# Optimization experiments

Measured on AMD Instinct MI355X. Metric: run time of the kernel, lower is better.

The kernel has to match this reference:

```python
import jax, jax.numpy as jnp
import numpy as np

HEADS = 8
TOK = 4  # num_query_tokens
EPS = 1e-5


def _ln(x, w, b):
    mu = jnp.mean(x, -1, keepdims=True)
    v = jnp.var(x, -1, keepdims=True)
    return (x - mu) / jnp.sqrt(v + EPS) * w + b


def _inorm(x):
    # InstanceNorm3d(affine=False): normalize per (B,C) over spatial dims
    mu = jnp.mean(x, (2, 3, 4), keepdims=True)
    v = jnp.var(x, (2, 3, 4), keepdims=True)
    return (x - mu) / jnp.sqrt(v + EPS)


def _conv3(x, w, b):
    y = jax.lax.conv_general_dilated(x, w, (1, 1, 1), 'SAME',
                                     dimension_numbers=('NCDHW', 'OIDHW', 'NCDHW'))
    return y + b[None, :, None, None, None]


def setup_inputs() -> dict:
    key = jax.random.key(0)
    ks = jax.random.split(key, 8)
    B, C, D, H, W = 4, 320, 16, 32, 32
    CLI = 320
    QD = C * TOK  # 1280
    s = 0.02
    return {
        'img_feat': jax.random.normal(ks[0], (B, C, D, H, W), jnp.float32),
        'cli_feat': jax.random.normal(ks[1], (B, CLI), jnp.float32),
        'Wq': jax.random.normal(ks[2], (QD, CLI), jnp.float32) * s,
        'bq': jnp.zeros((QD,), jnp.float32),
        'lnq_w': jnp.ones((QD,), jnp.float32),
        'lnq_b': jnp.zeros((QD,), jnp.float32),
        'Wk': jax.random.normal(ks[3], (C, C), jnp.float32) * s,
        'bk': jnp.zeros((C,), jnp.float32),
        'Wv': jax.random.normal(ks[4], (C, C), jnp.float32) * s,
        'bv': jnp.zeros((C,), jnp.float32),
        'Wo': jax.random.normal(ks[5], (C, QD), jnp.float32) * s,
        'bo': jnp.zeros((C,), jnp.float32),
        'lno_w': jnp.ones((C,), jnp.float32),
        'lno_b': jnp.zeros((C,), jnp.float32),
        'Wf1': jax.random.normal(ks[6], (C, 2 * C, 3, 3, 3), jnp.float32) * s,
        'bf1': jnp.zeros((C,), jnp.float32),
        'Wf2': jax.random.normal(ks[7], (C, C, 3, 3, 3), jnp.float32) * s,
        'bf2': jnp.zeros((C,), jnp.float32),
    }


def reference(img_feat, cli_feat, Wq, bq, lnq_w, lnq_b, Wk, bk, Wv, bv,
              Wo, bo, lno_w, lno_b, Wf1, bf1, Wf2, bf2):
    B, C, D, H, W = img_feat.shape
    S = D * H * W
    hd = C // HEADS
    scale = hd ** -0.5
    # clinical features -> 4 query tokens per head: [B, heads, head_dim, TOK]
    q = _ln(cli_feat @ Wq.T + bq, lnq_w, lnq_b).reshape(B, HEADS, hd, TOK)
    # 1x1x1 convs == per-position linear over channels
    x = img_feat.reshape(B, C, S)
    k = (jnp.einsum('oc,bcs->bos', Wk, x) + bk[None, :, None]).reshape(B, HEADS, hd, S)
    v = (jnp.einsum('oc,bcs->bos', Wv, x) + bv[None, :, None]).reshape(B, HEADS, hd, S)
    # [B, heads, TOK, S] scores -> softmax over spatial
    attn = jax.nn.softmax(jnp.einsum('bhdt,bhds->bhts', q, k) * scale, axis=-1)
    # value @ attn^T -> [B, heads, head_dim, TOK], flatten like torch .view(B,-1)
    o = jnp.einsum('bhds,bhts->bhdt', v, attn).reshape(B, HEADS * hd * TOK)
    o = _ln(o @ Wo.T + bo, lno_w, lno_b)  # [B, C]
    bcast = jnp.broadcast_to(o[:, :, None, None, None], (B, C, D, H, W))
    fused = jnp.concatenate([img_feat, bcast], axis=1)  # [B, 2C, D, H, W]
    h = jax.nn.gelu(_inorm(_conv3(fused, Wf1, bf1)), approximate=False)
    h = _inorm(_conv3(h, Wf2, bf2))
    return h + img_feat
```

## Files before the change

kernel.cpp:

```cpp
#include <hip/hip_runtime.h>
#include <hip/hip_bf16.h>
#include <math.h>

typedef unsigned short u16;

#define DEV static __device__ __forceinline__

DEV float bfu(u16 u) { union { unsigned int i; float f; } v; v.i = ((unsigned int)u) << 16; return v.f; }
DEV u16 fbu(float f) { __hip_bfloat16 h = __float2bfloat16(f); return *reinterpret_cast<u16*>(&h); }

template <typename T> struct ModeOf;
template <> struct ModeOf<u16>   { static constexpr int v = 0; };
template <> struct ModeOf<float> { static constexpr int v = 1; };
template <typename T> DEV float ld(const void* p, size_t i);
template <> DEV float ld<u16>(const void* p, size_t i)   { return bfu(((const u16*)p)[i]); }
template <> DEV float ld<float>(const void* p, size_t i) { return ((const float*)p)[i]; }

template <typename T> DEV float dot8(const void* img, size_t idx, const float* ar, int s);
template <> DEV float dot8<u16>(const void* img, size_t idx, const float* ar, int s) {
    uint4 v = *reinterpret_cast<const uint4*>((const u16*)img + idx + s);
    const float4 a0 = *reinterpret_cast<const float4*>(ar + s);
    const float4 a1 = *reinterpret_cast<const float4*>(ar + s + 4);
    return a0.x*bfu(v.x & 0xffff) + a0.y*bfu(v.x >> 16)
         + a0.z*bfu(v.y & 0xffff) + a0.w*bfu(v.y >> 16)
         + a1.x*bfu(v.z & 0xffff) + a1.y*bfu(v.z >> 16)
         + a1.z*bfu(v.w & 0xffff) + a1.w*bfu(v.w >> 16);
}
template <> DEV float dot8<float>(const void* img, size_t idx, const float* ar, int s) {
    const float4 x0 = *reinterpret_cast<const float4*>((const float*)img + idx + s);
    const float4 x1 = *reinterpret_cast<const float4*>((const float*)img + idx + s + 4);
    const float4 a0 = *reinterpret_cast<const float4*>(ar + s);
    const float4 a1 = *reinterpret_cast<const float4*>(ar + s + 4);
    return a0.x*x0.x + a0.y*x0.y + a0.z*x0.z + a0.w*x0.w
         + a1.x*x1.x + a1.y*x1.y + a1.z*x1.z + a1.w*x1.w;
}

#define NB 4
#define NC 320
#define ND 16
#define NH 32
#define NW 32
#define NS 16384
#define NHD 40
#define NQD 1280
#define NR 32
#define NTOK 4
#define OUT_N (NB*NC*NS)
#define EPSV 1e-5f
#define SCALE 0.15811388300841898f

#define YKS 8
#define YCH (NS / YKS)

#define CSL 32
#define NSL 10
#define HALO_D 4
#define HALO_H 6
#define PIXW 34
#define NPIX (HALO_D*HALO_H*PIXW)
#define PACKN (27*10*20*64*8)

typedef __attribute__((ext_vector_type(8))) short bf16x8;
typedef __attribute__((ext_vector_type(4))) float f32x4;

DEV int swz4(int p) { return (p + (p >> 2)) & 3; }

DEV float blk_sum(float v, float* red) {
    __syncthreads();
#pragma unroll
    for (int o = 32; o > 0; o >>= 1) v += __shfl_down(v, o, 64);
    int wv = threadIdx.x >> 6, ln = threadIdx.x & 63;
    if (ln == 0) red[wv] = v;
    __syncthreads();
    return red[0] + red[1] + red[2] + red[3];
}
DEV float blk_max(float v, float* red) {
    __syncthreads();
#pragma unroll
    for (int o = 32; o > 0; o >>= 1) v = fmaxf(v, __shfl_down(v, o, 64));
    int wv = threadIdx.x >> 6, ln = threadIdx.x & 63;
    if (ln == 0) red[wv] = v;
    __syncthreads();
    return fmaxf(fmaxf(red[0], red[1]), fmaxf(red[2], red[3]));
}

__global__ void detect_kernel(const u16* __restrict__ lnqw, int* __restrict__ flag) {
    if (threadIdx.x == 0) flag[0] = (lnqw[0] == 0x3F80) ? 0 : 1;
}

template <typename T>
__global__ __launch_bounds__(256) void q_kernel(const int* __restrict__ flag,
        const void* __restrict__ cli, const void* __restrict__ Wq, const void* __restrict__ bq,
        const void* __restrict__ lnw, const void* __restrict__ lnb, float* __restrict__ qout) {
    if (*flag != ModeOf<T>::v) return;
    int b = blockIdx.x, tid = threadIdx.x;
    __shared__ float cl[NC];
    __shared__ float red[8];
    for (int i = tid; i < NC; i += 256) cl[i] = ld<T>(cli, b * NC + i);
    __syncthreads();
    float loc[5];
    float s1 = 0.f, s2 = 0.f;
#pragma unroll
    for (int k = 0; k < 5; ++k) {
        int j = tid + k * 256;
        float a = ld<T>(bq, j);
        size_t wr = (size_t)j * NC;
        for (int c = 0; c < NC; ++c) a += cl[c] * ld<T>(Wq, wr + c);
        loc[k] = a; s1 += a; s2 += a * a;
    }
    s1 = blk_sum(s1, red);
    s2 = blk_sum(s2, red);
    float mu = s1 / (float)NQD;
    float var = fmaxf(s2 / (float)NQD - mu * mu, 0.f);
    float rs = rsqrtf(var + EPSV);
#pragma unroll
    for (int k = 0; k < 5; ++k) {
        int j = tid + k * 256;
        qout[(size_t)b * NQD + j] = (loc[k] - mu) * rs * ld<T>(lnw, j) + ld<T>(lnb, j);
    }
}

template <typename T>
__global__ __launch_bounds__(256) void qw_kernel(const int* __restrict__ flag,
        const float* __restrict__ q, const void* __restrict__ Wk, const void* __restrict__ bk,
        float* __restrict__ qW, float* __restrict__ qb, u16* __restrict__ qwb) {
    if (*flag != ModeOf<T>::v) return;
    int gid = blockIdx.x * 256 + threadIdx.x;
    if (gid < NB * NR * NC) {
        int c = gid % NC;
        int r = (gid / NC) % NR;
        int b = gid / (NC * NR);
        int h = r >> 2, t = r & 3;
        float a = 0.f;
        const float* qb_ = q + (size_t)b * NQD;
        for (int d = 0; d < NHD; ++d)
            a += qb_[(h * NHD + d) * NTOK + t] * ld<T>(Wk, (size_t)(h * NHD + d) * NC + c);
        qW[gid] = a;
        int kk = c >> 5, gg = (c >> 3) & 3, j = c & 7;
        int mf = r >> 4, lane = (gg << 4) | (r & 15);
        qwb[(((size_t)(b * 10 + kk) * 2 + mf) << 9) + (lane << 3) + j] = fbu(a);
    }
    if (gid < NB * NR) {
        int r = gid & 31, b = gid >> 5;
        int h = r >> 2, t = r & 3;
        float a = 0.f;
        const float* qb_ = q + (size_t)b * NQD;
        for (int d = 0; d < NHD; ++d)
            a += qb_[(h * NHD + d) * NTOK + t] * ld<T>(bk, h * NHD + d);
        qb[gid] = a;
    }
}

__global__ __launch_bounds__(256) void scores_mm_kernel(
        const u16* __restrict__ imgt, const u16* __restrict__ qwb,
        const float* __restrict__ qb, float* __restrict__ attn) {
    int b = blockIdx.y;
    int s0 = blockIdx.x * 256 + (threadIdx.x >> 6) * 64;
    int ln = threadIdx.x & 63;
    int col = ln & 15, g = ln >> 4;
    bf16x8 af[10][2];
    const u16* qa = qwb + (size_t)b * 10 * 2 * 512;
#pragma unroll
    for (int kk = 0; kk < 10; ++kk)
#pragma unroll
        for (int mf = 0; mf < 2; ++mf)
            af[kk][mf] = *reinterpret_cast<const bf16x8*>(qa + (((kk << 1) + mf) << 9) + (ln << 3));
    f32x4 acc[2][4];
#pragma unroll
    for (int mf = 0; mf < 2; ++mf)
#pragma unroll
        for (int nf = 0; nf < 4; ++nf) acc[mf][nf] = (f32x4){0.f, 0.f, 0.f, 0.f};
    const u16* xb = imgt + (size_t)b * NS * NC;
#pragma unroll
    for (int kk = 0; kk < 10; ++kk) {
#pragma unroll
        for (int nf = 0; nf < 4; ++nf) {
            bf16x8 bf = *reinterpret_cast<const bf16x8*>(
                xb + (size_t)(s0 + nf * 16 + col) * NC + kk * 32 + (g << 3));
#pragma unroll
            for (int mf = 0; mf < 2; ++mf)
                acc[mf][nf] = __builtin_amdgcn_mfma_f32_16x16x32_bf16(
                    af[kk][mf], bf, acc[mf][nf], 0, 0, 0);
        }
    }
#pragma unroll
    for (int mf = 0; mf < 2; ++mf)
#pragma unroll
        for (int nf = 0; nf < 4; ++nf)
#pragma unroll
            for (int r = 0; r < 4; ++r) {
                int row = mf * 16 + g * 4 + r;
                attn[((size_t)(b * NR + row) << 14) + s0 + nf * 16 + col] =
                    (acc[mf][nf][r] + qb[b * NR + row]) * SCALE;
            }
}

__global__ __launch_bounds__(256) void softmax_kernel(float* __restrict__ attn) {
    int row = blockIdx.x;
    float* rp = attn + ((size_t)row << 14);
    __shared__ float red[8];
    float m = -1e30f;
    for (int s = threadIdx.x; s < NS; s += 256) m = fmaxf(m, rp[s]);
    m = blk_max(m, red);
    float sum = 0.f;
    for (int s = threadIdx.x; s < NS; s += 256) {
        float e = expf(rp[s] - m);
        rp[s] = e; sum += e;
    }
    sum = blk_sum(sum, red);
    float inv = 1.f / sum;
    for (int s = threadIdx.x; s < NS; s += 256) rp[s] *= inv;
}

template <typename T>
__global__ __launch_bounds__(256) void y_kernel(const int* __restrict__ flag,
        const float* __restrict__ attn, const void* __restrict__ img, float* __restrict__ yp) {
    if (*flag != ModeOf<T>::v) return;
    int row = blockIdx.x;
    int ks  = blockIdx.y;
    int b = row >> 5;
    int wv = threadIdx.x >> 6, ln = threadIdx.x & 63;
    const float* ar = attn + ((size_t)row << 14) + ks * YCH;
    size_t xb = (size_t)b * NC * NS + ks * YCH;
    float* yout = yp + ((size_t)ks * NB * NR + row) * NC;
    for (int c = wv; c < NC; c += 4) {
        size_t xr = xb + ((size_t)c << 14);
        float p = 0.f;
#pragma unroll
        for (int it = 0; it < YCH / 512; ++it)
            p += dot8<T>(img, xr, ar, it * 512 + ln * 8);
#pragma unroll
        for (int o = 32; o > 0; o >>= 1) p += __shfl_down(p, o, 64);
        if (ln == 0) yout[c] = p;
    }
}

__global__ __launch_bounds__(256) void yred_kernel(const float* __restrict__ yp, float* __restrict__ y) {
    int i = blockIdx.x * 256 + threadIdx.x;
    if (i >= NB * NR * NC) return;
    float s = 0.f;
#pragma unroll
    for (int k = 0; k < YKS; ++k) s += yp[(size_t)k * NB * NR * NC + i];
    y[i] = s;
}

template <typename T>
__global__ __launch_bounds__(256) void o_kernel(const int* __restrict__ flag,
        const float* __restrict__ y, const void* __restrict__ Wv, const void* __restrict__ bv,
        const void* __restrict__ Wo, const void* __restrict__ bo,
        const void* __restrict__ lnw, const void* __restrict__ lnb, float* __restrict__ o2) {
    if (*flag != ModeOf<T>::v) return;
    int b = blockIdx.x, tid = threadIdx.x;
    __shared__ float yl[NR * NC];
    __shared__ float ol[NQD];
    __shared__ float red[8];
    for (int i = tid; i < NR * NC; i += 256) yl[i] = y[(size_t)b * NR * NC + i];
    __syncthreads();
#pragma unroll
    for (int k = 0; k < 5; ++k) {
        int i = tid + k * 256;
        int h = i / 160, rem = i - h * 160;
        int d = rem >> 2, t = rem & 3;
        int wr = h * NHD + d, r = h * NTOK + t;
        float a = ld<T>(bv, wr);
        size_t wvr = (size_t)wr * NC;
        const float* yr = yl + r * NC;
        for (int c = 0; c < NC; ++c) a += ld<T>(Wv, wvr + c) * yr[c];
        ol[i] = a;
    }
    __syncthreads();
    for (int j = tid; j < NC; j += 256) {
        float a = ld<T>(bo, j);
        size_t wor = (size_t)j * NQD;
        for (int i = 0; i < NQD; ++i) a += ld<T>(Wo, wor + i) * ol[i];
        yl[j] = a;
    }
    __syncthreads();
    float s1 = 0.f, s2 = 0.f;
    for (int j = tid; j < NC; j += 256) { float v = yl[j]; s1 += v; s2 += v * v; }
    s1 = blk_sum(s1, red);
    s2 = blk_sum(s2, red);
    float mu = s1 / (float)NC;
    float var = fmaxf(s2 / (float)NC - mu * mu, 0.f);
    float rs = rsqrtf(var + EPSV);
    for (int j = tid; j < NC; j += 256)
        o2[(size_t)b * NC + j] = (yl[j] - mu) * rs * ld<T>(lnw, j) + ld<T>(lnb, j);
}

template <typename T>
__global__ __launch_bounds__(256) void p_kernel(const int* __restrict__ flag,
        const float* __restrict__ o2, const void* __restrict__ Wf1, float* __restrict__ P) {
    if (*flag != ModeOf<T>::v) return;
    int o = blockIdx.x, b = blockIdx.y;
    int tid = threadIdx.x, wv = tid >> 6, ln = tid & 63;
    __shared__ float red[4 * 27];
    __shared__ float taps[27];
    float acc[27];
#pragma unroll
    for (int k = 0; k < 27; ++k) acc[k] = 0.f;
    for (int c = tid; c < NC; c += 256) {
        float oc = o2[(size_t)b * NC + c];
        size_t wp = ((size_t)o * 640 + 320 + c) * 27;
#pragma unroll
        for (int k = 0; k < 27; ++k) acc[k] += oc * ld<T>(Wf1, wp + k);
    }
#pragma unroll
    for (int k = 0; k < 27; ++k) {
        float v = acc[k];
#pragma unroll
        for (int off = 32; off > 0; off >>= 1) v += __shfl_down(v, off, 64);
        if (ln == 0) red[wv * 27 + k] = v;
    }
    __syncthreads();
    if (tid < 27) taps[tid] = red[tid] + red[27 + tid] + red[54 + tid] + red[81 + tid];
    __syncthreads();
    if (tid < 27) {
        int pd = tid / 9, ph = (tid / 3) % 3, pw = tid % 3;
        float s = 0.f;
        for (int kd = 0; kd < 3; ++kd) {
            if ((pd == 0 && kd == 0) || (pd == 2 && kd == 2)) continue;
            for (int kh = 0; kh < 3; ++kh) {
                if ((ph == 0 && kh == 0) || (ph == 2 && kh == 2)) continue;
                for (int kw = 0; kw < 3; ++kw) {
                    if ((pw == 0 && kw == 0) || (pw == 2 && kw == 2)) continue;
                    s += taps[kd * 9 + kh * 3 + kw];
                }
            }
        }
        P[(size_t)(b * NC + o) * 27 + tid] = s;
    }
}

template <typename T>
__global__ __launch_bounds__(256) void imgt_kernel(const int* __restrict__ flag,
        const void* __restrict__ img, u16* __restrict__ outT) {
    if (*flag != ModeOf<T>::v) return;
    int b = blockIdx.z, c0 = blockIdx.y << 5, s0 = blockIdx.x << 5;
    int r = threadIdx.x >> 3, c4 = (threadIdx.x & 7) << 2;
    __shared__ float tile[32][33];
#pragma unroll
    for (int j = 0; j < 4; ++j)
        tile[r][c4 + j] = ld<T>(img, ((size_t)(b * NC + c0 + r) << 14) + s0 + c4 + j);
    __syncthreads();
    u16* op = outT + ((size_t)b * NS + s0 + r) * NC + c0 + c4;
#pragma unroll
    for (int j = 0; j < 4; ++j) op[j] = fbu(tile[c4 + j][r]);
}

template <typename TW>
__global__ __launch_bounds__(256) void pack_kernel(const int* __restrict__ flag,
        const void* __restrict__ wgt, const void* __restrict__ bias,
        u16* __restrict__ wpack, float* __restrict__ biasf, int wic) {
    if (*flag != ModeOf<TW>::v) return;
    int gid = blockIdx.x * 256 + threadIdx.x;
    if (gid < NC) biasf[gid] = ld<TW>(bias, gid);
    int lane = gid & 63;
    int rest = gid >> 6;
    int obg = rest % 20;  rest /= 20;
    int t = rest % 27;    int cs = rest / 27;
    int o  = (obg << 4) + (lane & 15);
    int c0 = (cs << 5) + ((lane >> 4) << 3);
    u16* dst = wpack + (size_t)gid * 8;
#pragma unroll
    for (int j = 0; j < 8; ++j)
        dst[j] = fbu(ld<TW>(wgt, ((size_t)o * wic + c0 + j) * 27 + t));
}

__global__ __launch_bounds__(256, 3) void convmm_kernel(
        const u16* __restrict__ inT, const u16* __restrict__ wpack,
        const float* __restrict__ biasf, const float* __restrict__ Pp,
        u16* __restrict__ out) {
    int d0 = (blockIdx.x >> 3) << 1;
    int h0 = (blockIdx.x & 7) << 2;
    int ob = blockIdx.y;
    int b  = blockIdx.z;
    int tid = threadIdx.x;
    int wv = tid >> 6, ln = tid & 63;
    int col = ln & 15, g = ln >> 4;

    __shared__ __align__(16) u16 lin[NPIX * CSL];

    {
        float4 z = {0.f, 0.f, 0.f, 0.f};
        float4* lp = reinterpret_cast<float4*>(lin);
        for (int i = tid; i < NPIX * CSL / 8; i += 256) lp[i] = z;
    }
    __syncthreads();

    f32x4 acc[4][4];
#pragma unroll
    for (int mi = 0; mi < 4; ++mi)
#pragma unroll
        for (int ni = 0; ni < 4; ++ni) acc[mi][ni] = (f32x4){0.f, 0.f, 0.f, 0.f};

    int pix0[4];
#pragma unroll
    for (int ni = 0; ni < 4; ++ni) {
        int nb = (wv << 2) + ni;
        int r2 = nb >> 1;
        int ddo = r2 >> 2, hho = r2 & 3;
        pix0[ni] = (ddo * HALO_H + hho) * PIXW + ((nb & 1) << 4) + col;
    }

    size_t inb = (size_t)b * NS * NC;

    for (int cs = 0; cs < NSL; ++cs) {
        for (int k = wv; k < 48; k += 4) {
            int hf = k & 1, rr = k >> 1;
            int dd = rr / HALO_H, hh = rr - dd * HALO_H;
            int dg = d0 + dd - 1, hg = h0 + hh - 1;
            if ((unsigned)dg < ND && (unsigned)hg < NH) {
                int pixbase = (dd * HALO_H + hh) * PIXW + 1 + (hf << 4);
                int p = pixbase + (ln >> 2);
                int wpos = (hf << 4) + (ln >> 2);
                int cg = (ln & 3) ^ swz4(p);
                const u16* src = inT + inb + ((size_t)(dg << 10) + (hg << 5) + wpos) * NC
                                 + (cs << 5) + (cg << 3);
                __builtin_amdgcn_global_load_lds(
                    (const __attribute__((address_space(1))) unsigned int*)src,
                    (__attribute__((address_space(3))) unsigned int*)(lin + pixbase * CSL),
                    16, 0, 0);
            }
        }
        __syncthreads();

        const u16* wp = wpack + (size_t)cs * 27 * 20 * 512;
#pragma unroll
        for (int t = 0; t < 27; ++t) {
            const int kd = t / 9, kh = (t / 3) % 3, kw = t % 3;
            bf16x8 af[4];
#pragma unroll
            for (int mi = 0; mi < 4; ++mi)
                af[mi] = *reinterpret_cast<const bf16x8*>(
                    wp + ((size_t)(t * 20 + (ob << 2) + mi) << 9) + (ln << 3));
            bf16x8 bfr[4];
#pragma unroll
            for (int ni = 0; ni < 4; ++ni) {
                int p = pix0[ni] + (kd * HALO_H + kh) * PIXW + kw;
                bfr[ni] = *reinterpret_cast<const bf16x8*>(
                    lin + p * CSL + ((g ^ swz4(p)) << 3));
            }
#pragma unroll
            for (int mi = 0; mi < 4; ++mi)
#pragma unroll
                for (int ni = 0; ni < 4; ++ni)
                    acc[mi][ni] = __builtin_amdgcn_mfma_f32_16x16x32_bf16(
                        af[mi], bfr[ni], acc[mi][ni], 0, 0, 0);
        }
        __syncthreads();
    }

#pragma unroll
    for (int ni = 0; ni < 4; ++ni) {
        int nb = (wv << 2) + ni;
        int r2 = nb >> 1;
        int d = d0 + (r2 >> 2);
        int h = h0 + (r2 & 3);
        int w = ((nb & 1) << 4) + col;
        int pd = (d == 0) ? 0 : ((d == ND - 1) ? 2 : 1);
        int ph = (h == 0) ? 0 : ((h == NH - 1) ? 2 : 1);
        int pw = (w == 0) ? 0 : ((w == NW - 1) ? 2 : 1);
        size_t sidx = ((size_t)d << 10) + (h << 5) + w;
#pragma unroll
        for (int mi = 0; mi < 4; ++mi) {
#pragma unroll
            for (int r = 0; r < 4; ++r) {
                int o = (ob << 6) + (mi << 4) + (g << 2) + r;
                float v = acc[mi][ni][r] + biasf[o];
                if (Pp) v += Pp[(size_t)(b * NC + o) * 27 + pd * 9 + ph * 3 + pw];
                out[((size_t)(b * NC + o) << 14) + sidx] = fbu(v);
            }
        }
    }
}

__global__ __launch_bounds__(256) void stats_kernel(const u16* __restrict__ raw, float* __restrict__ mean,
                                                    float* __restrict__ rstd) {
    int bo = blockIdx.x;
    const u16* base = raw + ((size_t)bo << 14);
    __shared__ float red[8];
    float s1 = 0.f, s2 = 0.f;
    for (int s0 = threadIdx.x * 8; s0 < NS; s0 += 2048) {
        uint4 v = *reinterpret_cast<const uint4*>(base + s0);
        float x0 = bfu(v.x & 0xffff), x1 = bfu(v.x >> 16);
        float x2 = bfu(v.y & 0xffff), x3 = bfu(v.y >> 16);
        float x4 = bfu(v.z & 0xffff), x5 = bfu(v.z >> 16);
        float x6 = bfu(v.w & 0xffff), x7 = bfu(v.w >> 16);
        s1 += ((x0 + x1) + (x2 + x3)) + ((x4 + x5) + (x6 + x7));
        s2 += ((x0*x0 + x1*x1) + (x2*x2 + x3*x3)) + ((x4*x4 + x5*x5) + (x6*x6 + x7*x7));
    }
    s1 = blk_sum(s1, red);
    s2 = blk_sum(s2, red);
    if (threadIdx.x == 0) {
        float mu = s1 / (float)NS;
        float var = fmaxf(s2 / (float)NS - mu * mu, 0.f);
        mean[bo] = mu;
        rstd[bo] = rsqrtf(var + EPSV);
    }
}

__global__ __launch_bounds__(256) void norm1t_kernel(const u16* __restrict__ raw,
        const float* __restrict__ mean, const float* __restrict__ rstd, u16* __restrict__ h1t) {
    int b = blockIdx.z, c0 = blockIdx.y << 5, s0 = blockIdx.x << 5;
    int r = threadIdx.x >> 3, c4 = (threadIdx.x & 7) << 2;
    __shared__ float tile[32][33];
    int bo = b * NC + c0 + r;
    float mu = mean[bo], rs = rstd[bo];
    const u16* rp = raw + ((size_t)bo << 14) + s0 + c4;
#pragma unroll
    for (int j = 0; j < 4; ++j) {
        float xn = (bfu(rp[j]) - mu) * rs;
        tile[r][c4 + j] = 0.5f * xn * (1.f + erff(xn * 0.70710678118654752f));
    }
    __syncthreads();
    u16* op = h1t + ((size_t)b * NS + s0 + r) * NC + c0 + c4;
#pragma unroll
    for (int j = 0; j < 4; ++j) op[j] = fbu(tile[c4 + j][r]);
}

template <typename T>
__global__ __launch_bounds__(256) void final_kernel(const int* __restrict__ flag,
        const u16* __restrict__ raw, const float* __restrict__ mean, const float* __restrict__ rstd,
        const void* __restrict__ img, void* __restrict__ outp) {
    if (*flag != ModeOf<T>::v) return;
    int idx = (blockIdx.x * 256 + threadIdx.x) * 4;
    if (idx >= OUT_N) return;
    int bo = idx >> 14;
    float mu = mean[bo], rs = rstd[bo];
    ushort4 rv = *reinterpret_cast<const ushort4*>(raw + idx);
    float r0 = (bfu(rv.x) - mu) * rs;
    float r1 = (bfu(rv.y) - mu) * rs;
    float r2 = (bfu(rv.z) - mu) * rs;
    float r3 = (bfu(rv.w) - mu) * rs;
    if (ModeOf<T>::v == 0) {
        ushort4 iv = *reinterpret_cast<const ushort4*>((const u16*)img + idx);
        ushort4 ov;
        ov.x = fbu(r0 + bfu(iv.x)); ov.y = fbu(r1 + bfu(iv.y));
        ov.z = fbu(r2 + bfu(iv.z)); ov.w = fbu(r3 + bfu(iv.w));
        *reinterpret_cast<ushort4*>((u16*)outp + idx) = ov;
    } else {
        float4 iv = *reinterpret_cast<const float4*>((const float*)img + idx);
        float4 ov = make_float4(r0 + iv.x, r1 + iv.y, r2 + iv.z, r3 + iv.w);
        *reinterpret_cast<float4*>((float*)outp + idx) = ov;
    }
}

extern "C" void kernel_launch(void* const* d_in, const int* in_sizes, int n_in,
                              void* d_out, int out_size, void* d_ws, size_t ws_size,
                              hipStream_t stream) {
    const void* IMG  = d_in[0];
    const void* CLI  = d_in[1];
    const void* WQ   = d_in[2];
    const void* BQ   = d_in[3];
    const void* LNQW = d_in[4];
    const void* LNQB = d_in[5];
    const void* WK   = d_in[6];
    const void* BK   = d_in[7];
    const void* WV   = d_in[8];
    const void* BV   = d_in[9];
    const void* WO   = d_in[10];
    const void* BO   = d_in[11];
    const void* LNOW = d_in[12];
    const void* LNOB = d_in[13];
    const void* WF1  = d_in[14];
    const void* BF1  = d_in[15];
    const void* WF2  = d_in[16];
    const void* BF2  = d_in[17];

    char* ws = (char*)d_ws;
    size_t off = 0;
    auto alloc = [&](size_t bytes) { void* p = ws + off; off += (bytes + 255) & ~(size_t)255; return p; };
    int*   FLAG  = (int*)  alloc(256);
    u16*   RAW   = (u16*)  alloc((size_t)OUT_N * 2);
    float* Qf    = (float*)alloc((size_t)NB * NQD * 4);
    float* QW    = (float*)alloc((size_t)NB * NR * NC * 4);
    float* QB    = (float*)alloc((size_t)NB * NR * 4);
    u16*   QWB   = (u16*)  alloc((size_t)NB * 10 * 2 * 512 * 2);
    float* Yb    = (float*)alloc((size_t)NB * NR * NC * 4);
    float* O2    = (float*)alloc((size_t)NB * NC * 4);
    float* PB    = (float*)alloc((size_t)NB * NC * 27 * 4);
    float* MEAN  = (float*)alloc((size_t)NB * NC * 4);
    float* RSTD  = (float*)alloc((size_t)NB * NC * 4);
    u16*   WPACK = (u16*)  alloc((size_t)PACKN * 2);
    float* BIASF = (float*)alloc((size_t)NC * 4);
    float* YP    = (float*)RAW;
    float* ATTN  = (float*)((char*)RAW + (16u << 20));
    u16*   IMGT  = (u16*)d_out;
    u16*   H1    = (u16*)d_out;
    (void)ws_size; (void)n_in; (void)in_sizes; (void)out_size;

    detect_kernel<<<1, 64, 0, stream>>>((const u16*)LNQW, FLAG);

    imgt_kernel<u16>  <<<dim3(512, 10, NB), 256, 0, stream>>>(FLAG, IMG, IMGT);
    imgt_kernel<float><<<dim3(512, 10, NB), 256, 0, stream>>>(FLAG, IMG, IMGT);

    q_kernel<u16>  <<<NB, 256, 0, stream>>>(FLAG, CLI, WQ, BQ, LNQW, LNQB, Qf);
    q_kernel<float><<<NB, 256, 0, stream>>>(FLAG, CLI, WQ, BQ, LNQW, LNQB, Qf);

    int qwg = (NB * NR * NC + 255) / 256;
    qw_kernel<u16>  <<<qwg, 256, 0, stream>>>(FLAG, Qf, WK, BK, QW, QB, QWB);
    qw_kernel<float><<<qwg, 256, 0, stream>>>(FLAG, Qf, WK, BK, QW, QB, QWB);

    scores_mm_kernel<<<dim3(64, NB), 256, 0, stream>>>(IMGT, QWB, QB, ATTN);

    softmax_kernel<<<NB * NR, 256, 0, stream>>>(ATTN);

    y_kernel<u16>  <<<dim3(NB * NR, YKS), 256, 0, stream>>>(FLAG, ATTN, IMG, YP);
    y_kernel<float><<<dim3(NB * NR, YKS), 256, 0, stream>>>(FLAG, ATTN, IMG, YP);

    yred_kernel<<<(NB * NR * NC + 255) / 256, 256, 0, stream>>>(YP, Yb);

    o_kernel<u16>  <<<NB, 256, 0, stream>>>(FLAG, Yb, WV, BV, WO, BO, LNOW, LNOB, O2);
    o_kernel<float><<<NB, 256, 0, stream>>>(FLAG, Yb, WV, BV, WO, BO, LNOW, LNOB, O2);

    p_kernel<u16>  <<<dim3(NC, NB), 256, 0, stream>>>(FLAG, O2, WF1, PB);
    p_kernel<float><<<dim3(NC, NB), 256, 0, stream>>>(FLAG, O2, WF1, PB);

    int pkg = (PACKN / 8 + 255) / 256;
    pack_kernel<u16>  <<<pkg, 256, 0, stream>>>(FLAG, WF1, BF1, WPACK, BIASF, 640);
    pack_kernel<float><<<pkg, 256, 0, stream>>>(FLAG, WF1, BF1, WPACK, BIASF, 640);

    convmm_kernel<<<dim3(64, 5, NB), 256, 0, stream>>>(IMGT, WPACK, BIASF, PB, RAW);

    stats_kernel<<<NB * NC, 256, 0, stream>>>(RAW, MEAN, RSTD);
    norm1t_kernel<<<dim3(512, 10, NB), 256, 0, stream>>>(RAW, MEAN, RSTD, H1);

    pack_kernel<u16>  <<<pkg, 256, 0, stream>>>(FLAG, WF2, BF2, WPACK, BIASF, 320);
    pack_kernel<float><<<pkg, 256, 0, stream>>>(FLAG, WF2, BF2, WPACK, BIASF, 320);

    convmm_kernel<<<dim3(64, 5, NB), 256, 0, stream>>>(H1, WPACK, BIASF, nullptr, RAW);

    stats_kernel<<<NB * NC, 256, 0, stream>>>(RAW, MEAN, RSTD);

    final_kernel<u16>  <<<(OUT_N / 4 + 255) / 256, 256, 0, stream>>>(FLAG, RAW, MEAN, RSTD, IMG, d_out);
    final_kernel<float><<<(OUT_N / 4 + 255) / 256, 256, 0, stream>>>(FLAG, RAW, MEAN, RSTD, IMG, d_out);
}
```

Measured before the change: 2.055 ms.

## Split softmax, use MFMA for attention-weighted sum, fuse norm stats into conv

Softmax is split into a parallel partial max/sum pass, a combine pass and a finalize pass that also writes a bf16 copy of the attention. The bf16 path then computes the attention-weighted channel sum with MFMA instead of scalar dot products. The separate per-channel stats kernels after each conv are removed: the conv epilogue accumulates sum and sum of squares via shuffles and atomics. This trades extra atomics and a bf16 rounding of the attention weights for fewer full passes over the conv outputs and better parallelism in softmax.

New measurement: 2.144 ms. 4.3% more time.

```diff
diff --git a/kernel.cpp b/kernel.cpp
--- a/kernel.cpp
+++ b/kernel.cpp
@@ -16,19 +16,9 @@
 template <> DEV float ld<u16>(const void* p, size_t i)   { return bfu(((const u16*)p)[i]); }
 template <> DEV float ld<float>(const void* p, size_t i) { return ((const float*)p)[i]; }
 
-template <typename T> DEV float dot8(const void* img, size_t idx, const float* ar, int s);
-template <> DEV float dot8<u16>(const void* img, size_t idx, const float* ar, int s) {
-    uint4 v = *reinterpret_cast<const uint4*>((const u16*)img + idx + s);
-    const float4 a0 = *reinterpret_cast<const float4*>(ar + s);
-    const float4 a1 = *reinterpret_cast<const float4*>(ar + s + 4);
-    return a0.x*bfu(v.x & 0xffff) + a0.y*bfu(v.x >> 16)
-         + a0.z*bfu(v.y & 0xffff) + a0.w*bfu(v.y >> 16)
-         + a1.x*bfu(v.z & 0xffff) + a1.y*bfu(v.z >> 16)
-         + a1.z*bfu(v.w & 0xffff) + a1.w*bfu(v.w >> 16);
-}
-template <> DEV float dot8<float>(const void* img, size_t idx, const float* ar, int s) {
-    const float4 x0 = *reinterpret_cast<const float4*>((const float*)img + idx + s);
-    const float4 x1 = *reinterpret_cast<const float4*>((const float*)img + idx + s + 4);
+DEV float dot8f(const float* img, size_t idx, const float* ar, int s) {
+    const float4 x0 = *reinterpret_cast<const float4*>(img + idx + s);
+    const float4 x1 = *reinterpret_cast<const float4*>(img + idx + s + 4);
     const float4 a0 = *reinterpret_cast<const float4*>(ar + s);
     const float4 a1 = *reinterpret_cast<const float4*>(ar + s + 4);
     return a0.x*x0.x + a0.y*x0.y + a0.z*x0.z + a0.w*x0.w
@@ -51,6 +41,8 @@
 
 #define YKS 8
 #define YCH (NS / YKS)
+#define YKC 32
+#define YCS (NS / YKC)
 
 #define CSL 32
 #define NSL 10
@@ -195,21 +187,82 @@
             }
 }
 
-__global__ __launch_bounds__(256) void softmax_kernel(float* __restrict__ attn) {
-    int row = blockIdx.x;
-    float* rp = attn + ((size_t)row << 14);
+__global__ __launch_bounds__(256) void smax_part_kernel(const float* __restrict__ attn,
+        float* __restrict__ pm, float* __restrict__ pl) {
+    int row = blockIdx.x, kc = blockIdx.y;
+    const float* rp = attn + ((size_t)row << 14) + kc * 2048;
     __shared__ float red[8];
-    float m = -1e30f;
-    for (int s = threadIdx.x; s < NS; s += 256) m = fmaxf(m, rp[s]);
+    int t4 = threadIdx.x * 4;
+    float4 v0 = *reinterpret_cast<const float4*>(rp + t4);
+    float4 v1 = *reinterpret_cast<const float4*>(rp + t4 + 1024);
+    float m = fmaxf(fmaxf(fmaxf(v0.x, v0.y), fmaxf(v0.z, v0.w)),
+                    fmaxf(fmaxf(v1.x, v1.y), fmaxf(v1.z, v1.w)));
     m = blk_max(m, red);
-    float sum = 0.f;
-    for (int s = threadIdx.x; s < NS; s += 256) {
-        float e = expf(rp[s] - m);
-        rp[s] = e; sum += e;
-    }
-    sum = blk_sum(sum, red);
-    float inv = 1.f / sum;
-    for (int s = threadIdx.x; s < NS; s += 256) rp[s] *= inv;
+    float s = expf(v0.x - m) + expf(v0.y - m) + expf(v0.z - m) + expf(v0.w - m)
+            + expf(v1.x - m) + expf(v1.y - m) + expf(v1.z - m) + expf(v1.w - m);
+    s = blk_sum(s, red);
+    if (threadIdx.x == 0) { pm[row * 8 + kc] = m; pl[row * 8 + kc] = s; }
+}
+
+__global__ __launch_bounds__(128) void smax_comb_kernel(const float* __restrict__ pm,
+        const float* __restrict__ pl, float* __restrict__ gm, float* __restrict__ gli) {
+    int row = threadIdx.x;
+    float M = -1e30f;
+#pragma unroll
+    for (int k = 0; k < 8; ++k) M = fmaxf(M, pm[row * 8 + k]);
+    float L = 0.f;
+#pragma unroll
+    for (int k = 0; k < 8; ++k) L += pl[row * 8 + k] * expf(pm[row * 8 + k] - M);
+    gm[row] = M; gli[row] = 1.f / L;
+}
+
+__global__ __launch_bounds__(256) void smax_fin_kernel(float* __restrict__ attn,
+        const float* __restrict__ gm, const float* __restrict__ gli, u16* __restrict__ attnb) {
+    int row = blockIdx.x, kc = blockIdx.y;
+    size_t base = ((size_t)row << 14) + kc * 2048;
+    float M = gm[row], LI = gli[row];
+    int t4 = threadIdx.x * 4;
+#pragma unroll
+    for (int h = 0; h < 2; ++h) {
+        size_t i = base + t4 + h * 1024;
+        float4 v = *reinterpret_cast<const float4*>(attn + i);
+        v.x = expf(v.x - M) * LI; v.y = expf(v.y - M) * LI;
+        v.z = expf(v.z - M) * LI; v.w = expf(v.w - M) * LI;
+        *reinterpret_cast<float4*>(attn + i) = v;
+        ushort4 bv; bv.x = fbu(v.x); bv.y = fbu(v.y); bv.z = fbu(v.z); bv.w = fbu(v.w);
+        *reinterpret_cast<ushort4*>(attnb + i) = bv;
+    }
+}
+
+__global__ __launch_bounds__(256) void ymm_kernel(const int* __restrict__ flag,
+        const u16* __restrict__ attnb, const void* __restrict__ img, float* __restrict__ yp) {
+    if (*flag != 0) return;
+    int kc = blockIdx.x, ct = blockIdx.y, b = blockIdx.z;
+    int wv = threadIdx.x >> 6, ln = threadIdx.x & 63;
+    int col = ln & 15, g = ln >> 4;
+    int s0 = kc * YCS;
+    const u16* imgB = (const u16*)img;
+    const u16* ap0 = attnb + (((size_t)b * 32 + col) << 14) + s0 + (g << 3);
+    const u16* bp  = imgB + (((size_t)(b * NC + ct * 64 + wv * 16 + col)) << 14) + s0 + (g << 3);
+    f32x4 acc[2];
+    acc[0] = (f32x4){0.f, 0.f, 0.f, 0.f};
+    acc[1] = (f32x4){0.f, 0.f, 0.f, 0.f};
+#pragma unroll
+    for (int ks = 0; ks < YCS / 32; ++ks) {
+        bf16x8 bf = *reinterpret_cast<const bf16x8*>(bp + ks * 32);
+        bf16x8 a0 = *reinterpret_cast<const bf16x8*>(ap0 + ks * 32);
+        bf16x8 a1 = *reinterpret_cast<const bf16x8*>(ap0 + (16 << 14) + ks * 32);
+        acc[0] = __builtin_amdgcn_mfma_f32_16x16x32_bf16(a0, bf, acc[0], 0, 0, 0);
+        acc[1] = __builtin_amdgcn_mfma_f32_16x16x32_bf16(a1, bf, acc[1], 0, 0, 0);
+    }
+    int c = ct * 64 + wv * 16 + col;
+#pragma unroll
+    for (int mf = 0; mf < 2; ++mf)
+#pragma unroll
+        for (int r = 0; r < 4; ++r) {
+            int row = b * 32 + mf * 16 + g * 4 + r;
+            yp[((size_t)kc * NB * NR + row) * NC + c] = acc[mf][r];
+        }
 }
 
 template <typename T>
@@ -228,19 +281,20 @@
         float p = 0.f;
 #pragma unroll
         for (int it = 0; it < YCH / 512; ++it)
-            p += dot8<T>(img, xr, ar, it * 512 + ln * 8);
+            p += dot8f((const float*)img, xr, ar, it * 512 + ln * 8);
 #pragma unroll
         for (int o = 32; o > 0; o >>= 1) p += __shfl_down(p, o, 64);
         if (ln == 0) yout[c] = p;
     }
 }
 
-__global__ __launch_bounds__(256) void yred_kernel(const float* __restrict__ yp, float* __restrict__ y) {
+__global__ __launch_bounds__(256) void yred_kernel(const int* __restrict__ flag, int mode, int nk,
+        const float* __restrict__ yp, float* __restrict__ y) {
+    if (*flag != mode) return;
     int i = blockIdx.x * 256 + threadIdx.x;
     if (i >= NB * NR * NC) return;
     float s = 0.f;
-#pragma unroll
-    for (int k = 0; k < YKS; ++k) s += yp[(size_t)k * NB * NR * NC + i];
+    for (int k = 0; k < nk; ++k) s += yp[(size_t)k * NB * NR * NC + i];
     y[i] = s;
 }
 
@@ -366,10 +420,15 @@
         dst[j] = fbu(ld<TW>(wgt, ((size_t)o * wic + c0 + j) * 27 + t));
 }
 
+__global__ __launch_bounds__(256) void zstats_kernel(float* __restrict__ s1, float* __restrict__ s2) {
+    int i = blockIdx.x * 256 + threadIdx.x;
+    if (i < NB * NC) { s1[i] = 0.f; s2[i] = 0.f; }
+}
+
 __global__ __launch_bounds__(256, 3) void convmm_kernel(
         const u16* __restrict__ inT, const u16* __restrict__ wpack,
         const float* __restrict__ biasf, const float* __restrict__ Pp,
-        u16* __restrict__ out) {
+        u16* __restrict__ out, float* __restrict__ S1, float* __restrict__ S2) {
     int d0 = (blockIdx.x >> 3) << 1;
     int h0 = (blockIdx.x & 7) << 2;
     int ob = blockIdx.y;
@@ -450,6 +509,7 @@
         __syncthreads();
     }
 
+    size_t sidxA[4]; int pofA[4];
 #pragma unroll
     for (int ni = 0; ni < 4; ++ni) {
         int nb = (wv << 2) + ni;
@@ -460,43 +520,44 @@
         int pd = (d == 0) ? 0 : ((d == ND - 1) ? 2 : 1);
         int ph = (h == 0) ? 0 : ((h == NH - 1) ? 2 : 1);
         int pw = (w == 0) ? 0 : ((w == NW - 1) ? 2 : 1);
-        size_t sidx = ((size_t)d << 10) + (h << 5) + w;
-#pragma unroll
-        for (int mi = 0; mi < 4; ++mi) {
-#pragma unroll
-            for (int r = 0; r < 4; ++r) {
-                int o = (ob << 6) + (mi << 4) + (g << 2) + r;
-                float v = acc[mi][ni][r] + biasf[o];
-                if (Pp) v += Pp[(size_t)(b * NC + o) * 27 + pd * 9 + ph * 3 + pw];
-                out[((size_t)(b * NC + o) << 14) + sidx] = fbu(v);
+        sidxA[ni] = ((size_t)d << 10) + (h << 5) + w;
+        pofA[ni] = pd * 9 + ph * 3 + pw;
+    }
+#pragma unroll
+    for (int mi = 0; mi < 4; ++mi) {
+#pragma unroll
+        for (int r = 0; r < 4; ++r) {
+            int o = (ob << 6) + (mi << 4) + (g << 2) + r;
+            float bs = biasf[o];
+            float s1 = 0.f, s2 = 0.f;
+#pragma unroll
+            for (int ni = 0; ni < 4; ++ni) {
+                float v = acc[mi][ni][r] + bs;
+                if (Pp) v += Pp[(size_t)(b * NC + o) * 27 + pofA[ni]];
+                out[((size_t)(b * NC + o) << 14) + sidxA[ni]] = fbu(v);
+                s1 += v; s2 += v * v;
+            }
+#pragma unroll
+            for (int m = 1; m < 16; m <<= 1) {
+                s1 += __shfl_xor(s1, m, 64);
+                s2 += __shfl_xor(s2, m, 64);
+            }
+            if (col == 0) {
+                atomicAdd(&S1[b * NC + o], s1);
+                atomicAdd(&S2[b * NC + o], s2);
             }
         }
     }
 }
 
-__global__ __launch_bounds__(256) void stats_kernel(const u16* __restrict__ raw, float* __restrict__ mean,
-                                                    float* __restrict__ rstd) {
-    int bo = blockIdx.x;
-    const u16* base = raw + ((size_t)bo << 14);
-    __shared__ float red[8];
-    float s1 = 0.f, s2 = 0.f;
-    for (int s0 = threadIdx.x * 8; s0 < NS; s0 += 2048) {
-        uint4 v = *reinterpret_cast<const uint4*>(base + s0);
-        float x0 = bfu(v.x & 0xffff), x1 = bfu(v.x >> 16);
-        float x2 = bfu(v.y & 0xffff), x3 = bfu(v.y >> 16);
-        float x4 = bfu(v.z & 0xffff), x5 = bfu(v.z >> 16);
-        float x6 = bfu(v.w & 0xffff), x7 = bfu(v.w >> 16);
-        s1 += ((x0 + x1) + (x2 + x3)) + ((x4 + x5) + (x6 + x7));
-        s2 += ((x0*x0 + x1*x1) + (x2*x2 + x3*x3)) + ((x4*x4 + x5*x5) + (x6*x6 + x7*x7));
-    }
-    s1 = blk_sum(s1, red);
-    s2 = blk_sum(s2, red);
-    if (threadIdx.x == 0) {
-        float mu = s1 / (float)NS;
-        float var = fmaxf(s2 / (float)NS - mu * mu, 0.f);
-        mean[bo] = mu;
-        rstd[bo] = rsqrtf(var + EPSV);
-    }
+__global__ __launch_bounds__(256) void statsfin_kernel(const float* __restrict__ S1,
+        const float* __restrict__ S2, float* __restrict__ mean, float* __restrict__ rstd) {
+    int i = blockIdx.x * 256 + threadIdx.x;
+    if (i >= NB * NC) return;
+    float mu = S1[i] / (float)NS;
+    float var = fmaxf(S2[i] / (float)NS - mu * mu, 0.f);
+    mean[i] = mu;
+    rstd[i] = rsqrtf(var + EPSV);
 }
 
 __global__ __launch_bounds__(256) void norm1t_kernel(const u16* __restrict__ raw,
@@ -581,10 +642,17 @@
     float* PB    = (float*)alloc((size_t)NB * NC * 27 * 4);
     float* MEAN  = (float*)alloc((size_t)NB * NC * 4);
     float* RSTD  = (float*)alloc((size_t)NB * NC * 4);
+    float* ST1   = (float*)alloc((size_t)NB * NC * 4);
+    float* ST2   = (float*)alloc((size_t)NB * NC * 4);
+    float* PM    = (float*)alloc((size_t)NB * NR * 8 * 4);
+    float* PL    = (float*)alloc((size_t)NB * NR * 8 * 4);
+    float* GM    = (float*)alloc((size_t)NB * NR * 4);
+    float* GLI   = (float*)alloc((size_t)NB * NR * 4);
     u16*   WPACK = (u16*)  alloc((size_t)PACKN * 2);
     float* BIASF = (float*)alloc((size_t)NC * 4);
     float* YP    = (float*)RAW;
     float* ATTN  = (float*)((char*)RAW + (16u << 20));
+    u16*   ATTNB = (u16*)  ((char*)RAW + (26u << 20));
     u16*   IMGT  = (u16*)d_out;
     u16*   H1    = (u16*)d_out;
     (void)ws_size; (void)n_in; (void)in_sizes; (void)out_size;
@@ -603,12 +671,16 @@
 
     scores_mm_kernel<<<dim3(64, NB), 256, 0, stream>>>(IMGT, QWB, QB, ATTN);
 
-    softmax_kernel<<<NB * NR, 256, 0, stream>>>(ATTN);
-
-    y_kernel<u16>  <<<dim3(NB * NR, YKS), 256, 0, stream>>>(FLAG, ATTN, IMG, YP);
+    smax_part_kernel<<<dim3(NB * NR, 8), 256, 0, stream>>>(ATTN, PM, PL);
+    smax_comb_kernel<<<1, 128, 0, stream>>>(PM, PL, GM, GLI);
+    smax_fin_kernel<<<dim3(NB * NR, 8), 256, 0, stream>>>(ATTN, GM, GLI, ATTNB);
+
+    ymm_kernel<<<dim3(YKC, 5, NB), 256, 0, stream>>>(FLAG, ATTNB, IMG, YP);
     y_kernel<float><<<dim3(NB * NR, YKS), 256, 0, stream>>>(FLAG, ATTN, IMG, YP);
 
-    yred_kernel<<<(NB * NR * NC + 255) / 256, 256, 0, stream>>>(YP, Yb);
+    int yrg = (NB * NR * NC + 255) / 256;
+    yred_kernel<<<yrg, 256, 0, stream>>>(FLAG, 0, YKC, YP, Yb);
+    yred_kernel<<<yrg, 256, 0, stream>>>(FLAG, 1, YKS, YP, Yb);
 
     o_kernel<u16>  <<<NB, 256, 0, stream>>>(FLAG, Yb, WV, BV, WO, BO, LNOW, LNOB, O2);
     o_kernel<float><<<NB, 256, 0, stream>>>(FLAG, Yb, WV, BV, WO, BO, LNOW, LNOB, O2);
@@ -620,17 +692,18 @@
     pack_kernel<u16>  <<<pkg, 256, 0, stream>>>(FLAG, WF1, BF1, WPACK, BIASF, 640);
     pack_kernel<float><<<pkg, 256, 0, stream>>>(FLAG, WF1, BF1, WPACK, BIASF, 640);
 
-    convmm_kernel<<<dim3(64, 5, NB), 256, 0, stream>>>(IMGT, WPACK, BIASF, PB, RAW);
-
-    stats_kernel<<<NB * NC, 256, 0, stream>>>(RAW, MEAN, RSTD);
+    zstats_kernel<<<(NB * NC + 255) / 256, 256, 0, stream>>>(ST1, ST2);
+    convmm_kernel<<<dim3(64, 5, NB), 256, 0, stream>>>(IMGT, WPACK, BIASF, PB, RAW, ST1, ST2);
+    statsfin_kernel<<<(NB * NC + 255) / 256, 256, 0, stream>>>(ST1, ST2, MEAN, RSTD);
+
     norm1t_kernel<<<dim3(512, 10, NB), 256, 0, stream>>>(RAW, MEAN, RSTD, H1);
 
     pack_kernel<u16>  <<<pkg, 256, 0, stream>>>(FLAG, WF2, BF2, WPACK, BIASF, 320);
     pack_kernel<float><<<pkg, 256, 0, stream>>>(FLAG, WF2, BF2, WPACK, BIASF, 320);
 
-    convmm_kernel<<<dim3(64, 5, NB), 256, 0, stream>>>(H1, WPACK, BIASF, nullptr, RAW);
-
-    stats_kernel<<<NB * NC, 256, 0, stream>>>(RAW, MEAN, RSTD);
+    zstats_kernel<<<(NB * NC + 255) / 256, 256, 0, stream>>>(ST1, ST2);
+    convmm_kernel<<<dim3(64, 5, NB), 256, 0, stream>>>(H1, WPACK, BIASF, nullptr, RAW, ST1, ST2);
+    statsfin_kernel<<<(NB * NC + 255) / 256, 256, 0, stream>>>(ST1, ST2, MEAN, RSTD);
 
     final_kernel<u16>  <<<(OUT_N / 4 + 255) / 256, 256, 0, stream>>>(FLAG, RAW, MEAN, RSTD, IMG, d_out);
     final_kernel<float><<<(OUT_N / 4 + 255) / 256, 256, 0, stream>>>(FLAG, RAW, MEAN, RSTD, IMG, d_out);
```
